# Performance work log

Hardware: AMD Instinct MI355X
Metric: run time of the kernel (lower is better)

## Reference

```python
import jax, jax.numpy as jnp
import numpy as np

D, U, H = 3, 256, 8
DH = U // H
B, N, E = 128, 128, 512
BN_SCALE = 1.0 / np.sqrt(1.0 + 1e-3)  # keras BatchNorm inference with init moving stats (mean=0, var=1)


def setup_inputs() -> dict:
    key = jax.random.key(0)
    k = jax.random.split(key, 16)
    p = lambda kk, sh: jax.random.normal(kk, sh, jnp.float32) * 0.05
    return {
        "node_attr": jax.random.normal(k[0], (B, N, U), jnp.float32),
        "edge_attr": jax.random.normal(k[1], (B, E, U), jnp.float32),
        "edge_indices": jax.random.randint(k[2], (B, E, 2), 0, N, dtype=jnp.int32),
        "W_edge": p(k[3], (D, 3 * U, U)), "b_edge": jnp.zeros((D, U)),
        "gamma_e": jnp.ones((D, U)), "beta_e": jnp.zeros((D, U)),
        "W_node": p(k[4], (D, U, U)), "b_node": jnp.zeros((D, U)),
        "gamma_n": jnp.ones((D, U)), "beta_n": jnp.zeros((D, U)),
        "W_gat": p(k[5], (D, U, H, DH)), "a_gat": p(k[6], (D, H, 2 * DH + U)), "b_gat": jnp.zeros((D, H)),
        "W_gru": p(k[7], (D, U, 3 * U)), "U_gru": p(k[8], (D, U, 3 * U)), "b_gru": jnp.zeros((D, 3 * U)),
        "W_p1": p(k[9], (U, U)), "b_p1": jnp.zeros((U,)),
        "W_p2": p(k[10], (U, U // 2)), "b_p2": jnp.zeros((U // 2,)),
    }


def _bn(x, gamma, beta):
    # inference batchnorm with moving_mean=0, moving_var=1
    return x * (gamma * BN_SCALE) + beta


def _gather(nodes, idx):
    # nodes [B,N,F], idx [B,E] -> [B,E,F]
    return jnp.take_along_axis(nodes, idx[..., None], axis=1)


def _gat_one(h, eidx, edge, a, b):
    # h [N,H,DH], eidx [E,2], edge [E,U]; aggregate messages from src (col 1) at tgt (col 0)
    tgt, src = eidx[:, 0], eidx[:, 1]
    hi, hj = h[tgt], h[src]
    logit = (jnp.einsum('ehd,hd->eh', hi, a[:, :DH])
             + jnp.einsum('ehd,hd->eh', hj, a[:, DH:2 * DH])
             + edge @ a[:, 2 * DH:].T + b)
    logit = jax.nn.leaky_relu(logit, 0.2)
    # per-target-node segment softmax over variable-degree neighborhoods
    m = jnp.full((N, H), -1e9, logit.dtype).at[tgt].max(logit)
    ex = jnp.exp(logit - m[tgt])
    den = jnp.zeros((N, H), logit.dtype).at[tgt].add(ex) + 1e-9
    att = ex / den[tgt]
    out = jnp.zeros((N, H, DH), h.dtype).at[tgt].add(att[..., None] * hj)
    return out.reshape(N, H * DH)


def reference(node_attr, edge_attr, edge_indices, W_edge, b_edge, gamma_e, beta_e,
              W_node, b_node, gamma_n, beta_n, W_gat, a_gat, b_gat,
              W_gru, U_gru, b_gru, W_p1, b_p1, W_p2, b_p2):
    nodes, edges = node_attr, edge_attr
    tgt_idx = edge_indices[..., 0]
    src_idx = edge_indices[..., 1]
    for d in range(D):
        # edge update: gather endpoints, concat with edge feats, MLP, graph batchnorm
        e_in = _gather(nodes, src_idx)   # GatherNodesOutgoing
        e_out = _gather(nodes, tgt_idx)  # GatherNodesIngoing
        ec = jnp.concatenate([e_in, e_out, edges], axis=-1)  # [B,E,3U]
        e_up = _bn(jax.nn.relu(ec @ W_edge[d] + b_edge[d]), gamma_e[d], beta_e[d])
        # multi-head GAT attention over edges
        h = jnp.einsum('bnf,fhd->bnhd', nodes, W_gat[d])
        attended = jax.nn.relu(jax.vmap(_gat_one, in_axes=(0, 0, 0, None, None))(
            h, edge_indices, e_up, a_gat[d], b_gat[d]))
        # node MLP + batchnorm
        n_up = _bn(jax.nn.relu(nodes @ W_node[d] + b_node[d]), gamma_n[d], beta_n[d])
        # GRU update: state = n_up, input = attended
        xp = attended @ W_gru[d] + b_gru[d]
        hp = n_up @ U_gru[d]
        z = jax.nn.sigmoid(xp[..., :U] + hp[..., :U])
        r = jax.nn.sigmoid(xp[..., U:2 * U] + hp[..., U:2 * U])
        hh = jnp.tanh(xp[..., 2 * U:] + r * hp[..., 2 * U:])
        nodes = z * n_up + (1.0 - z) * hh
        edges = e_up
    emb = jnp.mean(nodes, axis=1)
    emb = jax.nn.relu(emb @ W_p1 + b_p1)
    emb = jax.nn.relu(emb @ W_p2 + b_p2)
    # inference-mode view augmentation is identity, so both views equal the base embedding
    views = jnp.stack([emb, emb], axis=1)  # [B, num_views, U//2]
    return emb, views
```

## Files before the change

### kernel.cpp

```cpp
#include <hip/hip_runtime.h>
#include <hip/hip_bf16.h>

constexpr int Dn  = 3;
constexpr int Un  = 256;
constexpr int Hn  = 8;
constexpr int DHn = 32;
constexpr int Bn  = 128;
constexpr int Nn  = 128;
constexpr int En  = 512;
constexpr float BN_SCALE_C = 0.9995003746877732f;

#define LB __launch_bounds__(256)
#define LB8 __launch_bounds__(512)

typedef short bf16x8 __attribute__((ext_vector_type(8)));
typedef unsigned short u16x8 __attribute__((ext_vector_type(8)));
typedef float f32x4 __attribute__((ext_vector_type(4)));
#define MFMA16(a, b, c) __builtin_amdgcn_mfma_f32_16x16x32_bf16(a, b, c, 0, 0, 0)

__device__ __forceinline__ void gload16(const void* g, void* l) {
  __builtin_amdgcn_global_load_lds(
      (const __attribute__((address_space(1))) void*)g,
      (__attribute__((address_space(3))) void*)l, 16, 0, 0);
}
__device__ __forceinline__ float sigm(float x) { return 1.f / (1.f + expf(-x)); }
__device__ __forceinline__ float bf2f(unsigned short u) {
  return __uint_as_float((unsigned)u << 16);
}

__global__ LB void k_f2bf(const float* __restrict__ in,
                          __hip_bfloat16* __restrict__ out, int n) {
  int i = (blockIdx.x * 256 + threadIdx.x) * 4;
  if (i + 3 < n) {
    float4 v = *reinterpret_cast<const float4*>(in + i);
    out[i + 0] = __float2bfloat16(v.x);
    out[i + 1] = __float2bfloat16(v.y);
    out[i + 2] = __float2bfloat16(v.z);
    out[i + 3] = __float2bfloat16(v.w);
  }
}

__global__ LB void k_prep_edge(const float* __restrict__ W,
                               __hip_bfloat16* __restrict__ Wt) {
  int idx = blockIdx.x * 256 + threadIdx.x;
  int d = idx / (Un * 3 * Un);
  int rem = idx % (Un * 3 * Un);
  int n = rem / (3 * Un);
  int k = rem % (3 * Un);
  Wt[idx] = __float2bfloat16(W[(size_t)d * 3 * Un * Un + (size_t)k * Un + n]);
}

__global__ LB void k_prep_hn(const float* __restrict__ Wg,
                             const float* __restrict__ Wn,
                             __hip_bfloat16* __restrict__ Wt) {
  int idx = blockIdx.x * 256 + threadIdx.x;
  int d = idx / (512 * 256);
  int rem = idx % (512 * 256);
  int n = rem / 256;
  int k = rem % 256;
  float v = (n < 256) ? Wg[(size_t)d * 65536 + k * 256 + n]
                      : Wn[(size_t)d * 65536 + k * 256 + (n - 256)];
  Wt[idx] = __float2bfloat16(v);
}

__global__ LB void k_prep_gru2(const float* __restrict__ W,
                               const float* __restrict__ U,
                               __hip_bfloat16* __restrict__ Wt) {
  int idx = blockIdx.x * 256 + threadIdx.x;
  int d = idx / (768 * 512);
  int rem = idx % (768 * 512);
  int j2 = rem >> 9;
  int k = rem & 511;
  const size_t wb = (size_t)d * 196608;
  float v = (k < 256) ? W[wb + k * 768 + j2] : U[wb + (k - 256) * 768 + j2];
  Wt[idx] = __float2bfloat16(v);
}

__global__ LB8 void k_edge_mfma(const __hip_bfloat16* __restrict__ nodes,
                                const __hip_bfloat16* __restrict__ edges,
                                const int* __restrict__ eidx,
                                const __hip_bfloat16* __restrict__ Wt,
                                const float* __restrict__ bias,
                                const float* __restrict__ gamma,
                                const float* __restrict__ beta,
                                __hip_bfloat16* __restrict__ e_up) {
  __shared__ __align__(16) short As[128 * 64];
  __shared__ __align__(16) short Bs[256 * 64];
  const int tid = threadIdx.x, lane = tid & 63;
  const int w = tid >> 6, wr = w >> 2, wc = w & 3;
  const int bid = blockIdx.x;
  const int wgid = (bid & 7) * 64 + (bid >> 3);
  const int row0 = wgid * 128;
  const __hip_bfloat16 *pa0[2], *pa1[2], *pa2[2], *pb[4];
  int sxa[2], sxb[4];
#pragma unroll
  for (int i = 0; i < 2; ++i) {
    int c = i * 512 + tid, row = c >> 3, slot = c & 7;
    int R = row0 + row, b = R >> 9, e = R & 511;
    int tt = eidx[(b * En + e) * 2 + 0];
    int ss = eidx[(b * En + e) * 2 + 1];
    pa0[i] = nodes + (size_t)(b * Nn + ss) * Un;
    pa1[i] = nodes + (size_t)(b * Nn + tt) * Un;
    pa2[i] = edges + (size_t)(b * En + e) * Un;
    sxa[i] = (slot ^ (row & 7)) * 8;
  }
#pragma unroll
  for (int i = 0; i < 4; ++i) {
    int c = i * 512 + tid, j = c >> 3, slot = c & 7;
    pb[i] = Wt + (size_t)j * 768;
    sxb[i] = (slot ^ (j & 7)) * 8;
  }
  f32x4 acc[4][4] = {};
  const int ldsb = (tid & 448) * 16;
  for (int kt = 0; kt < 768; kt += 64) {
    const int region = kt >> 8, koff = kt & 255;
#pragma unroll
    for (int i = 0; i < 2; ++i) {
      const __hip_bfloat16* s = (region == 0) ? pa0[i] : (region == 1 ? pa1[i] : pa2[i]);
      gload16(s + koff + sxa[i], (char*)As + i * 8192 + ldsb);
    }
#pragma unroll
    for (int i = 0; i < 4; ++i)
      gload16(pb[i] + kt + sxb[i], (char*)Bs + i * 8192 + ldsb);
    __syncthreads();
#pragma unroll
    for (int ks = 0; ks < 2; ++ks) {
      const int lc = ks * 4 + (lane >> 4);
      bf16x8 af[4], bfv[4];
#pragma unroll
      for (int mi = 0; mi < 4; ++mi) {
        int row = wr * 64 + mi * 16 + (lane & 15);
        af[mi] = *(const bf16x8*)((const char*)As + row * 128 + ((lc ^ (row & 7)) << 4));
      }
#pragma unroll
      for (int ni = 0; ni < 4; ++ni) {
        int col = wc * 64 + ni * 16 + (lane & 15);
        bfv[ni] = *(const bf16x8*)((const char*)Bs + col * 128 + ((lc ^ (col & 7)) << 4));
      }
#pragma unroll
      for (int mi = 0; mi < 4; ++mi)
#pragma unroll
        for (int ni = 0; ni < 4; ++ni)
          acc[mi][ni] = MFMA16(af[mi], bfv[ni], acc[mi][ni]);
    }
    __syncthreads();
  }
#pragma unroll
  for (int mi = 0; mi < 4; ++mi)
#pragma unroll
    for (int ni = 0; ni < 4; ++ni) {
      int C = wc * 64 + ni * 16 + (lane & 15);
      float gs = gamma[C] * BN_SCALE_C, bt = beta[C], bi = bias[C];
#pragma unroll
      for (int r = 0; r < 4; ++r) {
        int R = row0 + wr * 64 + mi * 16 + (lane >> 4) * 4 + r;
        float v = acc[mi][ni][r] + bi;
        v = fmaxf(v, 0.f) * gs + bt;
        e_up[(size_t)R * Un + C] = __float2bfloat16(v);
      }
    }
}

__global__ LB8 void k_hn_mfma(const __hip_bfloat16* __restrict__ A,
                              const __hip_bfloat16* __restrict__ Wt,
                              const float* __restrict__ nb,
                              const float* __restrict__ ng,
                              const float* __restrict__ nbe,
                              __hip_bfloat16* __restrict__ h_bf,
                              __hip_bfloat16* __restrict__ nupb) {
  __shared__ __align__(16) short As[128 * 64];
  __shared__ __align__(16) short Bs[256 * 64];
  const int tid = threadIdx.x, lane = tid & 63;
  const int w = tid >> 6, wr = w >> 2, wc = w & 3;
  const int bid = blockIdx.x;
  const int wgid = (bid & 7) * 32 + (bid >> 3);
  const int row0 = (wgid >> 1) * 128, col0 = (wgid & 1) * 256;
  const __hip_bfloat16 *pa[2], *pb[4];
  int sxa[2], sxb[4];
#pragma unroll
  for (int i = 0; i < 2; ++i) {
    int c = i * 512 + tid, row = c >> 3, slot = c & 7;
    pa[i] = A + (size_t)(row0 + row) * Un;
    sxa[i] = (slot ^ (row & 7)) * 8;
  }
#pragma unroll
  for (int i = 0; i < 4; ++i) {
    int c = i * 512 + tid, j = c >> 3, slot = c & 7;
    pb[i] = Wt + (size_t)(col0 + j) * Un;
    sxb[i] = (slot ^ (j & 7)) * 8;
  }
  f32x4 acc[4][4] = {};
  const int ldsb = (tid & 448) * 16;
  for (int kt = 0; kt < 256; kt += 64) {
#pragma unroll
    for (int i = 0; i < 2; ++i)
      gload16(pa[i] + kt + sxa[i], (char*)As + i * 8192 + ldsb);
#pragma unroll
    for (int i = 0; i < 4; ++i)
      gload16(pb[i] + kt + sxb[i], (char*)Bs + i * 8192 + ldsb);
    __syncthreads();
#pragma unroll
    for (int ks = 0; ks < 2; ++ks) {
      const int lc = ks * 4 + (lane >> 4);
      bf16x8 af[4], bfv[4];
#pragma unroll
      for (int mi = 0; mi < 4; ++mi) {
        int row = wr * 64 + mi * 16 + (lane & 15);
        af[mi] = *(const bf16x8*)((const char*)As + row * 128 + ((lc ^ (row & 7)) << 4));
      }
#pragma unroll
      for (int ni = 0; ni < 4; ++ni) {
        int col = wc * 64 + ni * 16 + (lane & 15);
        bfv[ni] = *(const bf16x8*)((const char*)Bs + col * 128 + ((lc ^ (col & 7)) << 4));
      }
#pragma unroll
      for (int mi = 0; mi < 4; ++mi)
#pragma unroll
        for (int ni = 0; ni < 4; ++ni)
          acc[mi][ni] = MFMA16(af[mi], bfv[ni], acc[mi][ni]);
    }
    __syncthreads();
  }
  const bool is_h = (col0 < 256);
#pragma unroll
  for (int mi = 0; mi < 4; ++mi)
#pragma unroll
    for (int ni = 0; ni < 4; ++ni) {
      int c2 = wc * 64 + ni * 16 + (lane & 15);
#pragma unroll
      for (int r = 0; r < 4; ++r) {
        int R = row0 + wr * 64 + mi * 16 + (lane >> 4) * 4 + r;
        float v = acc[mi][ni][r];
        if (is_h) {
          h_bf[(size_t)R * Un + c2] = __float2bfloat16(v);
        } else {
          v += nb[c2];
          v = fmaxf(v, 0.f) * (ng[c2] * BN_SCALE_C) + nbe[c2];
          nupb[(size_t)R * Un + c2] = __float2bfloat16(v);
        }
      }
    }
}

__global__ LB void k_gru_mfma2(const __hip_bfloat16* __restrict__ attb,
                               const __hip_bfloat16* __restrict__ nupb,
                               const __hip_bfloat16* __restrict__ Wt,
                               const float* __restrict__ bg,
                               __hip_bfloat16* __restrict__ nodes_out) {
  __shared__ __align__(16) short As[128 * 64];
  __shared__ __align__(16) short Bs[96 * 64];
  const int tid = threadIdx.x, lane = tid & 63;
  const int w = tid >> 6, wr = w >> 1, wc = w & 1;
  const int bid = blockIdx.x;
  const int wgid = (bid & 7) * 128 + (bid >> 3);
  const int row0 = (wgid >> 3) * 128, c0 = (wgid & 7) * 32;
  const __hip_bfloat16 *paA[4], *paN[4], *pb[3];
  int sxa[4], sxb[3];
#pragma unroll
  for (int i = 0; i < 4; ++i) {
    int c = i * 256 + tid, row = c >> 3, slot = c & 7;
    paA[i] = attb + (size_t)(row0 + row) * Un;
    paN[i] = nupb + (size_t)(row0 + row) * Un;
    sxa[i] = (slot ^ (row & 7)) * 8;
  }
#pragma unroll
  for (int i = 0; i < 3; ++i) {
    int l = i * 256 + tid, j = l >> 3, slot = l & 7;
    int grow = (j < 32) ? (c0 + j) : (j < 64) ? (256 + c0 + (j - 32))
                                              : (512 + c0 + (j - 64));
    pb[i] = Wt + (size_t)grow * 512;
    sxb[i] = (slot ^ (j & 7)) * 8;
  }
  f32x4 acc[4][4] = {};
  const int ldsb = (tid & 192) * 16;
  for (int kt = 0; kt < 512; kt += 64) {
    const int koff = kt & 255;
    const bool rA = kt < 256;
#pragma unroll
    for (int i = 0; i < 4; ++i) {
      const __hip_bfloat16* s = rA ? paA[i] : paN[i];
      gload16(s + koff + sxa[i], (char*)As + i * 4096 + ldsb);
    }
#pragma unroll
    for (int i = 0; i < 3; ++i)
      gload16(pb[i] + kt + sxb[i], (char*)Bs + i * 4096 + ldsb);
    __syncthreads();
    const int g2 = rA ? 2 : 3;
#pragma unroll
    for (int ks = 0; ks < 2; ++ks) {
      const int lc = ks * 4 + (lane >> 4);
      bf16x8 af[4], bv[3];
      const int jj = wc * 16 + (lane & 15);
      const int jsw = (lc ^ (jj & 7)) << 4;
      bv[0] = *(const bf16x8*)((const char*)Bs + jj * 128 + jsw);
      bv[1] = *(const bf16x8*)((const char*)Bs + (32 + jj) * 128 + jsw);
      bv[2] = *(const bf16x8*)((const char*)Bs + (64 + jj) * 128 + jsw);
#pragma unroll
      for (int mi = 0; mi < 4; ++mi) {
        int row = wr * 64 + mi * 16 + (lane & 15);
        af[mi] = *(const bf16x8*)((const char*)As + row * 128 + ((lc ^ (row & 7)) << 4));
      }
#pragma unroll
      for (int mi = 0; mi < 4; ++mi) {
        acc[0][mi] = MFMA16(af[mi], bv[0], acc[0][mi]);
        acc[1][mi] = MFMA16(af[mi], bv[1], acc[1][mi]);
        acc[g2][mi] = MFMA16(af[mi], bv[2], acc[g2][mi]);
      }
    }
    __syncthreads();
  }
  {
    const int c = c0 + wc * 16 + (lane & 15);
    const float bz = bg[c], br = bg[256 + c], bh = bg[512 + c];
    const unsigned short* nu_u = (const unsigned short*)nupb;
#pragma unroll
    for (int mi = 0; mi < 4; ++mi)
#pragma unroll
      for (int r = 0; r < 4; ++r) {
        int R = row0 + wr * 64 + mi * 16 + (lane >> 4) * 4 + r;
        float z  = sigm(acc[0][mi][r] + bz);
        float rr = sigm(acc[1][mi][r] + br);
        float hh = tanhf(acc[2][mi][r] + bh + rr * acc[3][mi][r]);
        float nu = bf2f(nu_u[(size_t)R * Un + c]);
        nodes_out[(size_t)R * Un + c] = __float2bfloat16(z * nu + (1.f - z) * hh);
      }
  }
}

__global__ LB void k_elog(const __hip_bfloat16* __restrict__ e_up,
                          const float* __restrict__ a_gat,
                          float* __restrict__ elog) {
  __shared__ float s_a[8][256];
  const int tid = threadIdx.x;
  for (int l = tid; l < 8 * 256; l += 256)
    s_a[l >> 8][l & 255] = a_gat[(l >> 8) * 320 + 64 + (l & 255)];
  __syncthreads();
  const int row = blockIdx.x * 64 + (tid >> 2);
  const int l4 = tid & 3;
  const u16x8* er = (const u16x8*)(e_up + (size_t)row * 256 + l4 * 64);
  float acc[8] = {};
#pragma unroll
  for (int c = 0; c < 8; ++c) {
    u16x8 v = er[c];
#pragma unroll
    for (int j = 0; j < 8; ++j) {
      float f = bf2f(v[j]);
      int k = l4 * 64 + c * 8 + j;
#pragma unroll
      for (int hh = 0; hh < 8; ++hh) acc[hh] += f * s_a[hh][k];
    }
  }
#pragma unroll
  for (int hh = 0; hh < 8; ++hh) {
    acc[hh] += __shfl_xor(acc[hh], 1);
    acc[hh] += __shfl_xor(acc[hh], 2);
  }
  elog[(size_t)row * 8 + 2 * l4]     = acc[2 * l4];
  elog[(size_t)row * 8 + 2 * l4 + 1] = acc[2 * l4 + 1];
}

__global__ LB void k_gat3(const __hip_bfloat16* __restrict__ h,
                          const float* __restrict__ elog,
                          const int* __restrict__ eidx,
                          const float* __restrict__ a_gat,
                          const float* __restrict__ b_gat,
                          __hip_bfloat16* __restrict__ att_bf) {
  const int b = blockIdx.x, hg = blockIdx.y;
  __shared__ int s_tgt[En], s_src[En];
  __shared__ float s_at[4][32], s_as[4][32];
  __shared__ float s_lt[Nn][4], s_ls[Nn][4];
  __shared__ float s_L[En][4];
  __shared__ int s_cnt[Nn], s_start[Nn], s_cur[Nn];
  __shared__ short s_ord[En];
  __shared__ float s_bg[4];
  __shared__ __align__(16) unsigned short hl[Nn][136];
  const int tid = threadIdx.x;
  if (tid < 4) s_bg[tid] = b_gat[hg * 4 + tid];
  if (tid < 128) {
    int q = tid >> 5, d = tid & 31;
    s_at[q][d] = a_gat[(hg * 4 + q) * 320 + d];
    s_as[q][d] = a_gat[(hg * 4 + q) * 320 + 32 + d];
  }
  for (int e = tid; e < En; e += 256) {
    s_tgt[e] = eidx[(b * En + e) * 2 + 0];
    s_src[e] = eidx[(b * En + e) * 2 + 1];
  }
  for (int l = tid; l < Nn; l += 256) s_cnt[l] = 0;
  for (int l = tid; l < En * 4; l += 256) {
    int e = l >> 2, q = l & 3;
    s_L[e][q] = elog[(size_t)(b * En + e) * 8 + hg * 4 + q];
  }
  const unsigned short* hu = (const unsigned short*)h;
  for (int l = tid; l < Nn * 16; l += 256) {
    int row = l >> 4, c8 = l & 15;
    u16x8 v = *(const u16x8*)(hu + (size_t)(b * Nn + row) * Un + hg * 128 + c8 * 8);
    *(u16x8*)&hl[row][c8 * 8] = v;
  }
  __syncthreads();
  for (int p = tid; p < Nn * 4; p += 256) {
    int n = p >> 2, q = p & 3;
    const unsigned short* hr = &hl[n][q * 32];
    float lt = 0.f, ls = 0.f;
#pragma unroll
    for (int c8 = 0; c8 < 4; ++c8) {
      u16x8 v = *(const u16x8*)(hr + c8 * 8);
#pragma unroll
      for (int j = 0; j < 8; ++j) {
        float f = bf2f(v[j]);
        int d = c8 * 8 + j;
        lt += f * s_at[q][d];
        ls += f * s_as[q][d];
      }
    }
    s_lt[n][q] = lt; s_ls[n][q] = ls;
  }
  for (int e = tid; e < En; e += 256) atomicAdd(&s_cnt[s_tgt[e]], 1);
  __syncthreads();
  if (tid == 0) {
    int acc = 0;
    for (int n = 0; n < Nn; ++n) { s_start[n] = acc; s_cur[n] = acc; acc += s_cnt[n]; }
  }
  __syncthreads();
  for (int e = tid; e < En; e += 256) {
    int pos = atomicAdd(&s_cur[s_tgt[e]], 1);
    s_ord[pos] = (short)e;
  }
  for (int l = tid; l < En * 4; l += 256) {
    int e = l >> 2, q = l & 3;
    float v = s_lt[s_tgt[e]][q] + s_ls[s_src[e]][q] + s_L[e][q] + s_bg[q];
    v = (v > 0.f) ? v : 0.2f * v;
    s_L[e][q] = v;
  }
  __syncthreads();
  for (int p = tid; p < Nn * 4; p += 256) {
    const int n = p >> 2, q = p & 3;
    const int st = s_start[n], cn = s_cnt[n];
    float m = -1e9f;
    for (int i = 0; i < cn; ++i) m = fmaxf(m, s_L[s_ord[st + i]][q]);
    float den = 1e-9f;
    for (int i = 0; i < cn; ++i) {
      const int e = s_ord[st + i];
      float ex = expf(s_L[e][q] - m);
      s_L[e][q] = ex;
      den += ex;
    }
    const float inv = 1.f / den;
    float acc[32] = {};
    for (int i = 0; i < cn; ++i) {
      const int e = s_ord[st + i];
      const float wgt = s_L[e][q] * inv;
      const unsigned short* hs = &hl[s_src[e]][q * 32];
#pragma unroll
      for (int c8 = 0; c8 < 4; ++c8) {
        u16x8 v = *(const u16x8*)(hs + c8 * 8);
#pragma unroll
        for (int j = 0; j < 8; ++j) acc[c8 * 8 + j] += wgt * bf2f(v[j]);
      }
    }
    __hip_bfloat16* ob = att_bf + (size_t)(b * Nn + n) * Un + (hg * 4 + q) * DHn;
#pragma unroll
    for (int d = 0; d < 32; ++d) ob[d] = __float2bfloat16(fmaxf(acc[d], 0.f));
  }
}

__global__ LB void k_pool(const __hip_bfloat16* __restrict__ nodes,
                          const float* __restrict__ Wp1, const float* __restrict__ bp1,
                          const float* __restrict__ Wp2, const float* __restrict__ bp2,
                          float* __restrict__ out) {
  const int b = blockIdx.x, tid = threadIdx.x;
  __shared__ float e0[256], e1[256];
  float s = 0.f;
  for (int n = 0; n < Nn; ++n) s += __bfloat162float(nodes[(size_t)(b * Nn + n) * Un + tid]);
  e0[tid] = s * (1.f / Nn);
  __syncthreads();
  float a1 = bp1[tid];
  for (int k = 0; k < 256; ++k) a1 += e0[k] * Wp1[k * 256 + tid];
  e1[tid] = fmaxf(a1, 0.f);
  __syncthreads();
  if (tid < 128) {
    float a2 = bp2[tid];
    for (int k = 0; k < 256; ++k) a2 += e1[k] * Wp2[k * 128 + tid];
    a2 = fmaxf(a2, 0.f);
    out[b * 128 + tid] = a2;
    out[Bn * 128 + b * 256 + tid] = a2;
    out[Bn * 128 + b * 256 + 128 + tid] = a2;
  }
}

extern "C" void kernel_launch(void* const* d_in, const int* in_sizes, int n_in,
                              void* d_out, int out_size, void* d_ws, size_t ws_size,
                              hipStream_t stream) {
  const float* node_attr = (const float*)d_in[0];
  const float* edge_attr = (const float*)d_in[1];
  const int*   eidx      = (const int*)d_in[2];
  const float* W_edge    = (const float*)d_in[3];
  const float* b_edge    = (const float*)d_in[4];
  const float* gamma_e   = (const float*)d_in[5];
  const float* beta_e    = (const float*)d_in[6];
  const float* W_node    = (const float*)d_in[7];
  const float* b_node    = (const float*)d_in[8];
  const float* gamma_n   = (const float*)d_in[9];
  const float* beta_n    = (const float*)d_in[10];
  const float* W_gat     = (const float*)d_in[11];
  const float* a_gat     = (const float*)d_in[12];
  const float* b_gat     = (const float*)d_in[13];
  const float* W_gru     = (const float*)d_in[14];
  const float* U_gru     = (const float*)d_in[15];
  const float* b_gru     = (const float*)d_in[16];
  const float* W_p1      = (const float*)d_in[17];
  const float* b_p1      = (const float*)d_in[18];
  const float* W_p2      = (const float*)d_in[19];
  const float* b_p2      = (const float*)d_in[20];

  char* p = (char*)d_ws;
  auto alloc = [&](size_t bytes) { char* q = p; p += (bytes + 255) & ~255ull; return q; };
  const size_t NODE_EL = (size_t)Bn * Nn * Un;
  const size_t EDGE_EL = (size_t)Bn * En * Un;
  __hip_bfloat16* nodes_bf = (__hip_bfloat16*)alloc(NODE_EL * 2);
  __hip_bfloat16* h_bf   = (__hip_bfloat16*)alloc(NODE_EL * 2);
  __hip_bfloat16* nup_bf = (__hip_bfloat16*)alloc(NODE_EL * 2);
  __hip_bfloat16* att_bf = (__hip_bfloat16*)alloc(NODE_EL * 2);
  float* elog   = (float*)alloc((size_t)Bn * En * 8 * 4);
  __hip_bfloat16* edges_a = (__hip_bfloat16*)alloc(EDGE_EL * 2);
  __hip_bfloat16* edges_b = (__hip_bfloat16*)alloc(EDGE_EL * 2);
  __hip_bfloat16* Wt_e   = (__hip_bfloat16*)alloc((size_t)Dn * 256 * 768 * 2);
  __hip_bfloat16* Wt_hn  = (__hip_bfloat16*)alloc((size_t)Dn * 512 * 256 * 2);
  __hip_bfloat16* Wt_gru = (__hip_bfloat16*)alloc((size_t)Dn * 768 * 512 * 2);

  k_f2bf<<<(int)(EDGE_EL / 1024), 256, 0, stream>>>(edge_attr, edges_a, (int)EDGE_EL);
  k_f2bf<<<(int)(NODE_EL / 1024), 256, 0, stream>>>(node_attr, nodes_bf, (int)NODE_EL);
  k_prep_edge<<<(Dn * 256 * 768) / 256, 256, 0, stream>>>(W_edge, Wt_e);
  k_prep_hn<<<(Dn * 512 * 256) / 256, 256, 0, stream>>>(W_gat, W_node, Wt_hn);
  k_prep_gru2<<<(Dn * 768 * 512) / 256, 256, 0, stream>>>(W_gru, U_gru, Wt_gru);

  __hip_bfloat16* ein = edges_a;
  __hip_bfloat16* eout = edges_b;
  for (int d = 0; d < Dn; ++d) {
    k_edge_mfma<<<512, 512, 0, stream>>>(
        nodes_bf, ein, eidx, Wt_e + (size_t)d * 256 * 768, b_edge + d * Un,
        gamma_e + d * Un, beta_e + d * Un, eout);
    k_hn_mfma<<<256, 512, 0, stream>>>(
        nodes_bf, Wt_hn + (size_t)d * 512 * 256, b_node + d * Un,
        gamma_n + d * Un, beta_n + d * Un, h_bf, nup_bf);
    k_elog<<<(Bn * En) / 64, 256, 0, stream>>>(
        eout, a_gat + (size_t)d * Hn * 320, elog);
    k_gat3<<<dim3(Bn, 2), 256, 0, stream>>>(
        h_bf, elog, eidx, a_gat + (size_t)d * Hn * 320, b_gat + d * Hn, att_bf);
    k_gru_mfma2<<<1024, 256, 0, stream>>>(
        att_bf, nup_bf, Wt_gru + (size_t)d * 768 * 512, b_gru + d * 3 * Un,
        nodes_bf);
    __hip_bfloat16* t = ein; ein = eout; eout = t;
  }
  k_pool<<<Bn, 256, 0, stream>>>(nodes_bf, W_p1, b_p1, W_p2, b_p2, (float*)d_out);
}
```

Before: 421.2 us.

## Merge edge, node-projection and edge-logit kernels into one launch

Combines the edge MLP GEMM and the node h/n_up GEMM into a single 768-block launch, with blocks dispatched by index, so the two independent GEMMs run concurrently and fill the GPU better. The edge-logit reduction is folded into the edge blocks' epilogue: each block re-reads its just-written e_up rows and computes the per-head edge logits, which removes a separate kernel and one launch. The epilogue relies on a block-level fence plus a barrier to see its own global writes, and the block must hold the a_gat slice in reused LDS, adding some tail work to the edge blocks.

Measured after the change: 445.0 us. 1.06x slower.

```diff
diff --git a/kernel.cpp b/kernel.cpp
--- a/kernel.cpp
+++ b/kernel.cpp
@@ -76,93 +76,17 @@
   Wt[idx] = __float2bfloat16(v);
 }
 
-__global__ LB8 void k_edge_mfma(const __hip_bfloat16* __restrict__ nodes,
-                                const __hip_bfloat16* __restrict__ edges,
-                                const int* __restrict__ eidx,
-                                const __hip_bfloat16* __restrict__ Wt,
-                                const float* __restrict__ bias,
-                                const float* __restrict__ gamma,
-                                const float* __restrict__ beta,
-                                __hip_bfloat16* __restrict__ e_up) {
-  __shared__ __align__(16) short As[128 * 64];
-  __shared__ __align__(16) short Bs[256 * 64];
-  const int tid = threadIdx.x, lane = tid & 63;
-  const int w = tid >> 6, wr = w >> 2, wc = w & 3;
-  const int bid = blockIdx.x;
-  const int wgid = (bid & 7) * 64 + (bid >> 3);
-  const int row0 = wgid * 128;
-  const __hip_bfloat16 *pa0[2], *pa1[2], *pa2[2], *pb[4];
-  int sxa[2], sxb[4];
-#pragma unroll
-  for (int i = 0; i < 2; ++i) {
-    int c = i * 512 + tid, row = c >> 3, slot = c & 7;
-    int R = row0 + row, b = R >> 9, e = R & 511;
-    int tt = eidx[(b * En + e) * 2 + 0];
-    int ss = eidx[(b * En + e) * 2 + 1];
-    pa0[i] = nodes + (size_t)(b * Nn + ss) * Un;
-    pa1[i] = nodes + (size_t)(b * Nn + tt) * Un;
-    pa2[i] = edges + (size_t)(b * En + e) * Un;
-    sxa[i] = (slot ^ (row & 7)) * 8;
-  }
-#pragma unroll
-  for (int i = 0; i < 4; ++i) {
-    int c = i * 512 + tid, j = c >> 3, slot = c & 7;
-    pb[i] = Wt + (size_t)j * 768;
-    sxb[i] = (slot ^ (j & 7)) * 8;
-  }
-  f32x4 acc[4][4] = {};
-  const int ldsb = (tid & 448) * 16;
-  for (int kt = 0; kt < 768; kt += 64) {
-    const int region = kt >> 8, koff = kt & 255;
-#pragma unroll
-    for (int i = 0; i < 2; ++i) {
-      const __hip_bfloat16* s = (region == 0) ? pa0[i] : (region == 1 ? pa1[i] : pa2[i]);
-      gload16(s + koff + sxa[i], (char*)As + i * 8192 + ldsb);
-    }
-#pragma unroll
-    for (int i = 0; i < 4; ++i)
-      gload16(pb[i] + kt + sxb[i], (char*)Bs + i * 8192 + ldsb);
-    __syncthreads();
-#pragma unroll
-    for (int ks = 0; ks < 2; ++ks) {
-      const int lc = ks * 4 + (lane >> 4);
-      bf16x8 af[4], bfv[4];
-#pragma unroll
-      for (int mi = 0; mi < 4; ++mi) {
-        int row = wr * 64 + mi * 16 + (lane & 15);
-        af[mi] = *(const bf16x8*)((const char*)As + row * 128 + ((lc ^ (row & 7)) << 4));
-      }
-#pragma unroll
-      for (int ni = 0; ni < 4; ++ni) {
-        int col = wc * 64 + ni * 16 + (lane & 15);
-        bfv[ni] = *(const bf16x8*)((const char*)Bs + col * 128 + ((lc ^ (col & 7)) << 4));
-      }
-#pragma unroll
-      for (int mi = 0; mi < 4; ++mi)
-#pragma unroll
-        for (int ni = 0; ni < 4; ++ni)
-          acc[mi][ni] = MFMA16(af[mi], bfv[ni], acc[mi][ni]);
-    }
-    __syncthreads();
-  }
-#pragma unroll
-  for (int mi = 0; mi < 4; ++mi)
-#pragma unroll
-    for (int ni = 0; ni < 4; ++ni) {
-      int C = wc * 64 + ni * 16 + (lane & 15);
-      float gs = gamma[C] * BN_SCALE_C, bt = beta[C], bi = bias[C];
-#pragma unroll
-      for (int r = 0; r < 4; ++r) {
-        int R = row0 + wr * 64 + mi * 16 + (lane >> 4) * 4 + r;
-        float v = acc[mi][ni][r] + bi;
-        v = fmaxf(v, 0.f) * gs + bt;
-        e_up[(size_t)R * Un + C] = __float2bfloat16(v);
-      }
-    }
-}
-
-__global__ LB8 void k_hn_mfma(const __hip_bfloat16* __restrict__ A,
-                              const __hip_bfloat16* __restrict__ Wt,
+__global__ LB8 void k_edge_hn(const __hip_bfloat16* __restrict__ nodes,
+                              const __hip_bfloat16* __restrict__ edges,
+                              const int* __restrict__ eidx,
+                              const __hip_bfloat16* __restrict__ Wt_e,
+                              const float* __restrict__ bias,
+                              const float* __restrict__ gamma,
+                              const float* __restrict__ beta,
+                              const float* __restrict__ a_gat,
+                              float* __restrict__ elog,
+                              __hip_bfloat16* __restrict__ e_up,
+                              const __hip_bfloat16* __restrict__ Wt_hn,
                               const float* __restrict__ nb,
                               const float* __restrict__ ng,
                               const float* __restrict__ nbe,
@@ -172,74 +96,178 @@
   __shared__ __align__(16) short Bs[256 * 64];
   const int tid = threadIdx.x, lane = tid & 63;
   const int w = tid >> 6, wr = w >> 2, wc = w & 3;
-  const int bid = blockIdx.x;
-  const int wgid = (bid & 7) * 32 + (bid >> 3);
-  const int row0 = (wgid >> 1) * 128, col0 = (wgid & 1) * 256;
-  const __hip_bfloat16 *pa[2], *pb[4];
-  int sxa[2], sxb[4];
-#pragma unroll
-  for (int i = 0; i < 2; ++i) {
-    int c = i * 512 + tid, row = c >> 3, slot = c & 7;
-    pa[i] = A + (size_t)(row0 + row) * Un;
-    sxa[i] = (slot ^ (row & 7)) * 8;
-  }
-#pragma unroll
-  for (int i = 0; i < 4; ++i) {
-    int c = i * 512 + tid, j = c >> 3, slot = c & 7;
-    pb[i] = Wt + (size_t)(col0 + j) * Un;
-    sxb[i] = (slot ^ (j & 7)) * 8;
-  }
-  f32x4 acc[4][4] = {};
-  const int ldsb = (tid & 448) * 16;
-  for (int kt = 0; kt < 256; kt += 64) {
-#pragma unroll
-    for (int i = 0; i < 2; ++i)
-      gload16(pa[i] + kt + sxa[i], (char*)As + i * 8192 + ldsb);
-#pragma unroll
-    for (int i = 0; i < 4; ++i)
-      gload16(pb[i] + kt + sxb[i], (char*)Bs + i * 8192 + ldsb);
+
+  if (blockIdx.x < 512) {
+    const int bid = blockIdx.x;
+    const int wgid = (bid & 7) * 64 + (bid >> 3);
+    const int row0 = wgid * 128;
+    const __hip_bfloat16 *pa0[2], *pa1[2], *pa2[2], *pb[4];
+    int sxa[2], sxb[4];
+#pragma unroll
+    for (int i = 0; i < 2; ++i) {
+      int c = i * 512 + tid, row = c >> 3, slot = c & 7;
+      int R = row0 + row, b = R >> 9, e = R & 511;
+      int tt = eidx[(b * En + e) * 2 + 0];
+      int ss = eidx[(b * En + e) * 2 + 1];
+      pa0[i] = nodes + (size_t)(b * Nn + ss) * Un;
+      pa1[i] = nodes + (size_t)(b * Nn + tt) * Un;
+      pa2[i] = edges + (size_t)(b * En + e) * Un;
+      sxa[i] = (slot ^ (row & 7)) * 8;
+    }
+#pragma unroll
+    for (int i = 0; i < 4; ++i) {
+      int c = i * 512 + tid, j = c >> 3, slot = c & 7;
+      pb[i] = Wt_e + (size_t)j * 768;
+      sxb[i] = (slot ^ (j & 7)) * 8;
+    }
+    f32x4 acc[4][4] = {};
+    const int ldsb = (tid & 448) * 16;
+    for (int kt = 0; kt < 768; kt += 64) {
+      const int region = kt >> 8, koff = kt & 255;
+#pragma unroll
+      for (int i = 0; i < 2; ++i) {
+        const __hip_bfloat16* s = (region == 0) ? pa0[i] : (region == 1 ? pa1[i] : pa2[i]);
+        gload16(s + koff + sxa[i], (char*)As + i * 8192 + ldsb);
+      }
+#pragma unroll
+      for (int i = 0; i < 4; ++i)
+        gload16(pb[i] + kt + sxb[i], (char*)Bs + i * 8192 + ldsb);
+      __syncthreads();
+#pragma unroll
+      for (int ks = 0; ks < 2; ++ks) {
+        const int lc = ks * 4 + (lane >> 4);
+        bf16x8 af[4], bfv[4];
+#pragma unroll
+        for (int mi = 0; mi < 4; ++mi) {
+          int row = wr * 64 + mi * 16 + (lane & 15);
+          af[mi] = *(const bf16x8*)((const char*)As + row * 128 + ((lc ^ (row & 7)) << 4));
+        }
+#pragma unroll
+        for (int ni = 0; ni < 4; ++ni) {
+          int col = wc * 64 + ni * 16 + (lane & 15);
+          bfv[ni] = *(const bf16x8*)((const char*)Bs + col * 128 + ((lc ^ (col & 7)) << 4));
+        }
+#pragma unroll
+        for (int mi = 0; mi < 4; ++mi)
+#pragma unroll
+          for (int ni = 0; ni < 4; ++ni)
+            acc[mi][ni] = MFMA16(af[mi], bfv[ni], acc[mi][ni]);
+      }
+      __syncthreads();
+    }
+#pragma unroll
+    for (int mi = 0; mi < 4; ++mi)
+#pragma unroll
+      for (int ni = 0; ni < 4; ++ni) {
+        int C = wc * 64 + ni * 16 + (lane & 15);
+        float gs = gamma[C] * BN_SCALE_C, bt = beta[C], bi = bias[C];
+#pragma unroll
+        for (int r = 0; r < 4; ++r) {
+          int R = row0 + wr * 64 + mi * 16 + (lane >> 4) * 4 + r;
+          float v = acc[mi][ni][r] + bi;
+          v = fmaxf(v, 0.f) * gs + bt;
+          e_up[(size_t)R * Un + C] = __float2bfloat16(v);
+        }
+      }
+    __threadfence_block();
+    float* s_a = (float*)As;
+    for (int l = tid; l < 8 * 256; l += 512)
+      s_a[l] = a_gat[(l >> 8) * 320 + 64 + (l & 255)];
     __syncthreads();
-#pragma unroll
-    for (int ks = 0; ks < 2; ++ks) {
-      const int lc = ks * 4 + (lane >> 4);
-      bf16x8 af[4], bfv[4];
-#pragma unroll
-      for (int mi = 0; mi < 4; ++mi) {
-        int row = wr * 64 + mi * 16 + (lane & 15);
-        af[mi] = *(const bf16x8*)((const char*)As + row * 128 + ((lc ^ (row & 7)) << 4));
-      }
+    {
+      const int row = row0 + (tid >> 2);
+      const int l4 = tid & 3;
+      const u16x8* er = (const u16x8*)(e_up + (size_t)row * 256 + l4 * 64);
+      float a2[8] = {};
+#pragma unroll
+      for (int c = 0; c < 8; ++c) {
+        u16x8 v = er[c];
+#pragma unroll
+        for (int j = 0; j < 8; ++j) {
+          float f = bf2f(v[j]);
+          int k = l4 * 64 + c * 8 + j;
+#pragma unroll
+          for (int hh = 0; hh < 8; ++hh) a2[hh] += f * s_a[hh * 256 + k];
+        }
+      }
+#pragma unroll
+      for (int hh = 0; hh < 8; ++hh) {
+        a2[hh] += __shfl_xor(a2[hh], 1);
+        a2[hh] += __shfl_xor(a2[hh], 2);
+      }
+      elog[(size_t)row * 8 + 2 * l4]     = a2[2 * l4];
+      elog[(size_t)row * 8 + 2 * l4 + 1] = a2[2 * l4 + 1];
+    }
+  } else {
+    const int bid = blockIdx.x - 512;
+    const int wgid = (bid & 7) * 32 + (bid >> 3);
+    const int row0 = (wgid >> 1) * 128, col0 = (wgid & 1) * 256;
+    const __hip_bfloat16 *pa[2], *pb[4];
+    int sxa[2], sxb[4];
+#pragma unroll
+    for (int i = 0; i < 2; ++i) {
+      int c = i * 512 + tid, row = c >> 3, slot = c & 7;
+      pa[i] = nodes + (size_t)(row0 + row) * Un;
+      sxa[i] = (slot ^ (row & 7)) * 8;
+    }
+#pragma unroll
+    for (int i = 0; i < 4; ++i) {
+      int c = i * 512 + tid, j = c >> 3, slot = c & 7;
+      pb[i] = Wt_hn + (size_t)(col0 + j) * Un;
+      sxb[i] = (slot ^ (j & 7)) * 8;
+    }
+    f32x4 acc[4][4] = {};
+    const int ldsb = (tid & 448) * 16;
+    for (int kt = 0; kt < 256; kt += 64) {
+#pragma unroll
+      for (int i = 0; i < 2; ++i)
+        gload16(pa[i] + kt + sxa[i], (char*)As + i * 8192 + ldsb);
+#pragma unroll
+      for (int i = 0; i < 4; ++i)
+        gload16(pb[i] + kt + sxb[i], (char*)Bs + i * 8192 + ldsb);
+      __syncthreads();
+#pragma unroll
+      for (int ks = 0; ks < 2; ++ks) {
+        const int lc = ks * 4 + (lane >> 4);
+        bf16x8 af[4], bfv[4];
+#pragma unroll
+        for (int mi = 0; mi < 4; ++mi) {
+          int row = wr * 64 + mi * 16 + (lane & 15);
+          af[mi] = *(const bf16x8*)((const char*)As + row * 128 + ((lc ^ (row & 7)) << 4));
+        }
+#pragma unroll
+        for (int ni = 0; ni < 4; ++ni) {
+          int col = wc * 64 + ni * 16 + (lane & 15);
+          bfv[ni] = *(const bf16x8*)((const char*)Bs + col * 128 + ((lc ^ (col & 7)) << 4));
+        }
+#pragma unroll
+        for (int mi = 0; mi < 4; ++mi)
+#pragma unroll
+          for (int ni = 0; ni < 4; ++ni)
+            acc[mi][ni] = MFMA16(af[mi], bfv[ni], acc[mi][ni]);
+      }
+      __syncthreads();
+    }
+    const bool is_h = (col0 < 256);
+#pragma unroll
+    for (int mi = 0; mi < 4; ++mi)
 #pragma unroll
       for (int ni = 0; ni < 4; ++ni) {
-        int col = wc * 64 + ni * 16 + (lane & 15);
-        bfv[ni] = *(const bf16x8*)((const char*)Bs + col * 128 + ((lc ^ (col & 7)) << 4));
-      }
-#pragma unroll
-      for (int mi = 0; mi < 4; ++mi)
-#pragma unroll
-        for (int ni = 0; ni < 4; ++ni)
-          acc[mi][ni] = MFMA16(af[mi], bfv[ni], acc[mi][ni]);
-    }
-    __syncthreads();
-  }
-  const bool is_h = (col0 < 256);
-#pragma unroll
-  for (int mi = 0; mi < 4; ++mi)
-#pragma unroll
-    for (int ni = 0; ni < 4; ++ni) {
-      int c2 = wc * 64 + ni * 16 + (lane & 15);
-#pragma unroll
-      for (int r = 0; r < 4; ++r) {
-        int R = row0 + wr * 64 + mi * 16 + (lane >> 4) * 4 + r;
-        float v = acc[mi][ni][r];
-        if (is_h) {
-          h_bf[(size_t)R * Un + c2] = __float2bfloat16(v);
-        } else {
-          v += nb[c2];
-          v = fmaxf(v, 0.f) * (ng[c2] * BN_SCALE_C) + nbe[c2];
-          nupb[(size_t)R * Un + c2] = __float2bfloat16(v);
-        }
-      }
-    }
+        int c2 = wc * 64 + ni * 16 + (lane & 15);
+#pragma unroll
+        for (int r = 0; r < 4; ++r) {
+          int R = row0 + wr * 64 + mi * 16 + (lane >> 4) * 4 + r;
+          float v = acc[mi][ni][r];
+          if (is_h) {
+            h_bf[(size_t)R * Un + c2] = __float2bfloat16(v);
+          } else {
+            v += nb[c2];
+            v = fmaxf(v, 0.f) * (ng[c2] * BN_SCALE_C) + nbe[c2];
+            nupb[(size_t)R * Un + c2] = __float2bfloat16(v);
+          }
+        }
+      }
+  }
 }
 
 __global__ LB void k_gru_mfma2(const __hip_bfloat16* __restrict__ attb,
@@ -325,38 +353,6 @@
         nodes_out[(size_t)R * Un + c] = __float2bfloat16(z * nu + (1.f - z) * hh);
       }
   }
-}
-
-__global__ LB void k_elog(const __hip_bfloat16* __restrict__ e_up,
-                          const float* __restrict__ a_gat,
-                          float* __restrict__ elog) {
-  __shared__ float s_a[8][256];
-  const int tid = threadIdx.x;
-  for (int l = tid; l < 8 * 256; l += 256)
-    s_a[l >> 8][l & 255] = a_gat[(l >> 8) * 320 + 64 + (l & 255)];
-  __syncthreads();
-  const int row = blockIdx.x * 64 + (tid >> 2);
-  const int l4 = tid & 3;
-  const u16x8* er = (const u16x8*)(e_up + (size_t)row * 256 + l4 * 64);
-  float acc[8] = {};
-#pragma unroll
-  for (int c = 0; c < 8; ++c) {
-    u16x8 v = er[c];
-#pragma unroll
-    for (int j = 0; j < 8; ++j) {
-      float f = bf2f(v[j]);
-      int k = l4 * 64 + c * 8 + j;
-#pragma unroll
-      for (int hh = 0; hh < 8; ++hh) acc[hh] += f * s_a[hh][k];
-    }
-  }
-#pragma unroll
-  for (int hh = 0; hh < 8; ++hh) {
-    acc[hh] += __shfl_xor(acc[hh], 1);
-    acc[hh] += __shfl_xor(acc[hh], 2);
-  }
-  elog[(size_t)row * 8 + 2 * l4]     = acc[2 * l4];
-  elog[(size_t)row * 8 + 2 * l4 + 1] = acc[2 * l4 + 1];
 }
 
 __global__ LB void k_gat3(const __hip_bfloat16* __restrict__ h,
@@ -536,14 +532,11 @@
   __hip_bfloat16* ein = edges_a;
   __hip_bfloat16* eout = edges_b;
   for (int d = 0; d < Dn; ++d) {
-    k_edge_mfma<<<512, 512, 0, stream>>>(
+    k_edge_hn<<<768, 512, 0, stream>>>(
         nodes_bf, ein, eidx, Wt_e + (size_t)d * 256 * 768, b_edge + d * Un,
-        gamma_e + d * Un, beta_e + d * Un, eout);
-    k_hn_mfma<<<256, 512, 0, stream>>>(
-        nodes_bf, Wt_hn + (size_t)d * 512 * 256, b_node + d * Un,
+        gamma_e + d * Un, beta_e + d * Un, a_gat + (size_t)d * Hn * 320, elog, eout,
+        Wt_hn + (size_t)d * 512 * 256, b_node + d * Un,
         gamma_n + d * Un, beta_n + d * Un, h_bf, nup_bf);
-    k_elog<<<(Bn * En) / 64, 256, 0, stream>>>(
-        eout, a_gat + (size_t)d * Hn * 320, elog);
     k_gat3<<<dim3(Bn, 2), 256, 0, stream>>>(
         h_bf, elog, eidx, a_gat + (size_t)d * Hn * 320, b_gat + d * Hn, att_bf);
     k_gru_mfma2<<<1024, 256, 0, stream>>>(
```
